# Optimization experiments

Measured on AMD Instinct MI355X. Metric: run time of the kernel, lower is better.

## Reference

```python
import jax, jax.numpy as jnp
import numpy as np

DIM = 1024
HEADS = 16
DEPTH = DIM // HEADS


def setup_inputs() -> dict:
    key = jax.random.key(0)
    ks = jax.random.split(key, 8)
    B, S = 4, 2048
    q = jax.random.normal(ks[0], (B, S, DIM), dtype=jnp.float32)
    k = jax.random.normal(ks[1], (B, S, DIM), dtype=jnp.float32)
    v = jax.random.normal(ks[2], (B, S, DIM), dtype=jnp.float32)
    # key-padding style mask: 1 = masked, 0 = attend; broadcasts over [B,H,S,S]
    mask = jax.random.randint(ks[3], (B, 1, 1, S), 0, 2).astype(jnp.float32)
    scale = 1.0 / np.sqrt(DIM)  # xavier_uniform-ish scale for square matrices
    WQ = jax.random.normal(ks[4], (DIM, DIM), dtype=jnp.float32) * scale
    WK = jax.random.normal(ks[5], (DIM, DIM), dtype=jnp.float32) * scale
    WV = jax.random.normal(ks[6], (DIM, DIM), dtype=jnp.float32) * scale
    WO = jax.random.normal(ks[7], (DIM, DIM), dtype=jnp.float32) * scale
    return {"q": q, "k": k, "v": v, "mask": mask, "WQ": WQ, "WK": WK, "WV": WV, "WO": WO}


def reference(q, k, v, mask, WQ, WK, WV, WO):
    B = q.shape[0]
    norm = jnp.asarray(np.sqrt(DEPTH), dtype=q.dtype)
    # projections -> [B,S,H,D]
    qh = (q @ WQ).reshape(B, -1, HEADS, DEPTH)
    kh = (k @ WK).reshape(B, -1, HEADS, DEPTH)
    vh = (v @ WV).reshape(B, -1, HEADS, DEPTH)
    # scores [B,H,Sq,Sk]
    g = jnp.einsum("bqhd,bkhd->bhqk", qh, kh) / norm
    g = g - mask * 1e9
    A = jax.nn.softmax(g, axis=-1)
    att = jnp.einsum("bhqk,bkhd->bqhd", A, vh).reshape(B, -1, DIM)
    return att @ WO
```

## Files before the change

### kernel.cpp

```cpp
#include <hip/hip_runtime.h>
#include <cstdint>
#include <cstddef>

#define DIM_   1024
#define HEADS_ 16
#define DEPTH_ 64
#define SEQ_   2048
#define BATCH_ 4
#define RCAP_  1152
#define NCH_   36

typedef __attribute__((ext_vector_type(8))) short short8;
typedef __attribute__((ext_vector_type(4))) float f32x4;
typedef _Float16 half8 __attribute__((ext_vector_type(8)));

__device__ __forceinline__ unsigned short f2bf(float x) {
    unsigned int u = __float_as_uint(x);
    u = u + 0x7FFFu + ((u >> 16) & 1u);
    return (unsigned short)(u >> 16);
}
__device__ __forceinline__ float bf2f(unsigned short h) {
    return __uint_as_float(((unsigned int)h) << 16);
}
__device__ __forceinline__ unsigned short f2h(float x) {
    _Float16 h = (_Float16)x;
    return __builtin_bit_cast(unsigned short, h);
}
__device__ __forceinline__ void async_cp16(const void* g, void* l) {
    __builtin_amdgcn_global_load_lds((const __attribute__((address_space(1))) void*)g,
                                     (__attribute__((address_space(3))) void*)l,
                                     16, 0, 0);
}

__global__ __launch_bounds__(64) void scan_mask(const float* __restrict__ mask,
                                                int* __restrict__ counts,
                                                int* __restrict__ idx) {
    const int b    = blockIdx.x;
    const int lane = threadIdx.x;
    const float* m = mask + (size_t)b * SEQ_;
    int* ib = idx + (size_t)b * SEQ_;
    int running = 0;
    for (int i0 = 0; i0 < SEQ_; i0 += 64) {
        const int i = i0 + lane;
        const bool keep = (m[i] == 0.0f);
        const unsigned long long bal = __ballot(keep);
        const int pre = __popcll(bal & ((1ULL << lane) - 1ULL));
        const int pos = running + pre;
        if (keep && pos < RCAP_) ib[pos] = i;
        running += __popcll(bal);
    }
    if (lane == 0) counts[b] = running < RCAP_ ? running : RCAP_;
}

__global__ __launch_bounds__(256) void convert_all(const float* __restrict__ q,
                                                   const float* __restrict__ k,
                                                   const float* __restrict__ v,
                                                   const float* __restrict__ WQ,
                                                   const float* __restrict__ WK,
                                                   const float* __restrict__ WV,
                                                   const float* __restrict__ WO,
                                                   const int* __restrict__ counts,
                                                   const int* __restrict__ idx,
                                                   unsigned short* __restrict__ qAh,
                                                   unsigned short* __restrict__ kAh,
                                                   unsigned short* __restrict__ vAh,
                                                   unsigned short* __restrict__ WhQ,
                                                   unsigned short* __restrict__ WhK,
                                                   unsigned short* __restrict__ WhV,
                                                   unsigned short* __restrict__ WhO) {
    const int bid = blockIdx.x;
    if (bid < 4096) {
        const int g  = bid * 256 + threadIdx.x;
        const int rb = g >> 14;
        const int w  = g & 16383;
        const int kt = w >> 9, x = w & 511;
        const int mtile = x >> 6, y = x & 63;
        const int kq = y >> 4, mm = y & 15;
        const int row   = rb * 128 + mtile * 16 + mm;
        const int kbase = kt * 32 + kq * 8;
        const float* src = q + (size_t)row * DIM_ + kbase;
        short8 vh;
#pragma unroll
        for (int j = 0; j < 8; ++j) vh[j] = (short)f2h(src[j]);
        *(short8*)(qAh + (size_t)g * 8) = vh;
    } else if (bid < 8704) {
        int lb = bid - 4096;
        const float* A;
        unsigned short* Ah;
        if (lb < 2304) { A = k; Ah = kAh; }
        else           { A = v; Ah = vAh; lb -= 2304; }
        const int g  = lb * 256 + threadIdx.x;
        const int rb = g >> 14;
        const int w  = g & 16383;
        const int kt = w >> 9, x = w & 511;
        const int mtile = x >> 6, y = x & 63;
        const int kq = y >> 4, mm = y & 15;
        const int b   = rb / 9;
        const int rbl = rb - b * 9;
        int r = rbl * 128 + mtile * 16 + mm;
        const int cnt = counts[b];
        if (r > cnt - 1) r = cnt - 1;
        const int rs = idx[b * SEQ_ + r];
        const int kbase = kt * 32 + kq * 8;
        const float* src = A + ((size_t)b * SEQ_ + rs) * DIM_ + kbase;
        short8 vh;
#pragma unroll
        for (int j = 0; j < 8; ++j) vh[j] = (short)f2h(src[j]);
        *(short8*)(Ah + (size_t)g * 8) = vh;
    } else {
        int lb = bid - 8704;
        const float* B;
        unsigned short* Bh;
        if (lb < 512)       { B = WQ; Bh = WhQ; }
        else if (lb < 1024) { B = WK; Bh = WhK; lb -= 512; }
        else if (lb < 1536) { B = WV; Bh = WhV; lb -= 1024; }
        else                { B = WO; Bh = WhO; lb -= 1536; }
        const int g  = lb * 256 + threadIdx.x;
        const int w  = g & 16383;
        const int kt = w >> 9, x = w & 511;
        const int nt = x >> 6, y = x & 63;
        const int kq = y >> 4, nn = y & 15;
        const int n  = nt * 16 + nn;
        const int nb = g >> 14;
        const int col = nb * 128 + n;
        const int k0 = kt * 32 + kq * 8;
        short8 vh;
#pragma unroll
        for (int j = 0; j < 8; ++j) vh[j] = (short)f2h(B[(size_t)(k0 + j) * DIM_ + col]);
        *(short8*)(Bh + (size_t)g * 8) = vh;
    }
}

__global__ __launch_bounds__(256) void gemm_qkv(const unsigned short* __restrict__ qAh,
                                                const unsigned short* __restrict__ kAh,
                                                const unsigned short* __restrict__ vAh,
                                                const unsigned short* __restrict__ WhQ,
                                                const unsigned short* __restrict__ WhK,
                                                const unsigned short* __restrict__ WhV,
                                                unsigned short* __restrict__ Qbf,
                                                unsigned short* __restrict__ Kswz,
                                                unsigned short* __restrict__ Vswz,
                                                const int* __restrict__ counts) {
    __shared__ unsigned short lds[2 * 8192];

    const int t = threadIdx.x, wave = t >> 6, lane = t & 63;
    const int x = blockIdx.x, cb = blockIdx.y;

    int mode, rb;
    const unsigned short *gA, *gB;
    unsigned short* C;
    if (x < 64)       { mode = 3; rb = x;       gA = qAh; gB = WhQ; C = Qbf; }
    else if (x < 100) { mode = 4; rb = x - 64;  gA = kAh; gB = WhK; C = Kswz; }
    else              { mode = 5; rb = x - 100; gA = vAh; gB = WhV; C = Vswz; }

    int cnt = 0, bb = 0;
    if (mode != 3) { bb = rb / 9; cnt = counts[bb]; }

    gA += (size_t)rb * 131072;
    gB += (size_t)cb * 131072;

    const int wr = wave >> 1, wc = wave & 1;

    f32x4 acc[4][4];
#pragma unroll
    for (int i = 0; i < 4; ++i)
#pragma unroll
        for (int j = 0; j < 4; ++j) acc[i][j] = (f32x4){0.f, 0.f, 0.f, 0.f};

    auto stage = [&](int kt, int sel) {
        const size_t ktO = (size_t)kt * 4096;
        char* lA = (char*)(lds + sel * 8192);
        char* lB = (char*)(lds + sel * 8192 + 4096);
#pragma unroll
        for (int i = 0; i < 2; ++i) {
            const int o = i * 4096 + t * 16;
            async_cp16((const char*)(gA + ktO) + o, lA + o);
            async_cp16((const char*)(gB + ktO) + o, lB + o);
        }
    };

    stage(0, 0);
    __syncthreads();
    int sel = 0;
    for (int kt = 0; kt < 32; ++kt) {
        if (kt < 31) stage(kt + 1, sel ^ 1);
        const unsigned short* lA = lds + sel * 8192;
        const unsigned short* lB = lA + 4096;

        half8 a[4], b[4];
#pragma unroll
        for (int i = 0; i < 4; ++i) {
            a[i] = *(const half8*)(lA + (wr * 4 + i) * 512 + lane * 8);
            b[i] = *(const half8*)(lB + (wc * 4 + i) * 512 + lane * 8);
        }
#pragma unroll
        for (int mt = 0; mt < 4; ++mt)
#pragma unroll
            for (int nt = 0; nt < 4; ++nt)
                acc[mt][nt] = __builtin_amdgcn_mfma_f32_16x16x32_f16(a[mt], b[nt], acc[mt][nt], 0, 0, 0);

        __syncthreads();
        sel ^= 1;
    }

    const int rq = lane >> 4, rc = lane & 15;
#pragma unroll
    for (int mt = 0; mt < 4; ++mt) {
#pragma unroll
        for (int nt = 0; nt < 4; ++nt) {
            const int col = cb * 128 + (wc * 4 + nt) * 16 + rc;
#pragma unroll
            for (int r = 0; r < 4; ++r) {
                const int row = rb * 128 + (wr * 4 + mt) * 16 + rq * 4 + r;
                const float val = acc[mt][nt][r];
                const int h = col >> 6, dd = col & (DEPTH_ - 1);
                if (mode == 3) {
                    const int b_ = row >> 11, s = row & (SEQ_ - 1);
                    C[((size_t)(b_ * HEADS_ + h) * SEQ_ + s) * DEPTH_ + dd] =
                        f2bf(val * 0.18033688011112042f);
                } else if (mode == 4) {
                    const int rl = row - bb * RCAP_;
                    const float sv = (rl < cnt) ? val : 0.f;
                    const size_t bh = (size_t)(bb * HEADS_ + h);
                    const size_t off = bh * (NCH_ * 2048)
                                     + (size_t)(rl >> 5) * 2048 + (size_t)((rl >> 4) & 1) * 1024
                                     + (size_t)(dd >> 5) * 512 + (size_t)((dd >> 3) & 3) * 128
                                     + (rl & 15) * 8 + (dd & 7);
                    C[off] = f2bf(sv);
                } else {
                    const int rl = row - bb * RCAP_;
                    const float sv = (rl < cnt) ? val : 0.f;
                    const size_t bh = (size_t)(bb * HEADS_ + h);
                    const size_t off = bh * (NCH_ * 2048)
                                     + (size_t)(rl >> 5) * 2048 + (size_t)(dd >> 4) * 512
                                     + (size_t)((rl >> 3) & 3) * 128
                                     + (dd & 15) * 8 + (rl & 7);
                    C[off] = f2bf(sv);
                }
            }
        }
    }
}

__global__ __launch_bounds__(256) void gemm_out(const unsigned short* __restrict__ Ah,
                                                const unsigned short* __restrict__ Bh,
                                                float* __restrict__ Cf) {
    __shared__ unsigned short lds[2 * 8192];

    const int t = threadIdx.x, wave = t >> 6, lane = t & 63;
    const int rb = blockIdx.x, cb = blockIdx.y;

    const unsigned short* gA = Ah + (size_t)rb * 131072;
    const unsigned short* gB = Bh + (size_t)cb * 131072;

    const int wr = wave >> 1, wc = wave & 1;

    f32x4 acc[4][4];
#pragma unroll
    for (int i = 0; i < 4; ++i)
#pragma unroll
        for (int j = 0; j < 4; ++j) acc[i][j] = (f32x4){0.f, 0.f, 0.f, 0.f};

    auto stage = [&](int kt, int sel) {
        const size_t ktO = (size_t)kt * 4096;
        char* lA = (char*)(lds + sel * 8192);
        char* lB = (char*)(lds + sel * 8192 + 4096);
#pragma unroll
        for (int i = 0; i < 2; ++i) {
            const int o = i * 4096 + t * 16;
            async_cp16((const char*)(gA + ktO) + o, lA + o);
            async_cp16((const char*)(gB + ktO) + o, lB + o);
        }
    };

    stage(0, 0);
    __syncthreads();
    int sel = 0;
    for (int kt = 0; kt < 32; ++kt) {
        if (kt < 31) stage(kt + 1, sel ^ 1);
        const unsigned short* lA = lds + sel * 8192;
        const unsigned short* lB = lA + 4096;

        half8 a[4], b[4];
#pragma unroll
        for (int i = 0; i < 4; ++i) {
            a[i] = *(const half8*)(lA + (wr * 4 + i) * 512 + lane * 8);
            b[i] = *(const half8*)(lB + (wc * 4 + i) * 512 + lane * 8);
        }
#pragma unroll
        for (int mt = 0; mt < 4; ++mt)
#pragma unroll
            for (int nt = 0; nt < 4; ++nt)
                acc[mt][nt] = __builtin_amdgcn_mfma_f32_16x16x32_f16(a[mt], b[nt], acc[mt][nt], 0, 0, 0);

        __syncthreads();
        sel ^= 1;
    }

    const int rq = lane >> 4, rc = lane & 15;
#pragma unroll
    for (int mt = 0; mt < 4; ++mt) {
#pragma unroll
        for (int nt = 0; nt < 4; ++nt) {
            const int col = cb * 128 + (wc * 4 + nt) * 16 + rc;
#pragma unroll
            for (int r = 0; r < 4; ++r) {
                const int row = rb * 128 + (wr * 4 + mt) * 16 + rq * 4 + r;
                Cf[(size_t)row * DIM_ + col] = acc[mt][nt][r];
            }
        }
    }
}

__global__ __launch_bounds__(256, 8) void attn_mfma(const unsigned short* __restrict__ Qbf,
                                                    const unsigned short* __restrict__ Kz,
                                                    const unsigned short* __restrict__ Vz,
                                                    const int* __restrict__ counts,
                                                    unsigned short* __restrict__ oAh) {
    __shared__ char lds[2 * 8192 + 4 * 1024];

    const int bh = blockIdx.x, qb = blockIdx.y;
    const int b = bh >> 4, h = bh & (HEADS_ - 1);
    const int t = threadIdx.x, wave = t >> 6, lane = t & 63;
    const int g = lane >> 4, n = lane & 15;
    const int cnt = counts[b];
    const int nch = (cnt + 31) >> 5;

    short8 qf[2];
    const int qrow0 = qb * 64 + wave * 16;
#pragma unroll
    for (int kf = 0; kf < 2; ++kf)
        qf[kf] = *(const short8*)(Qbf + ((size_t)bh * SEQ_ + qrow0 + n) * DEPTH_ + kf * 32 + g * 8);

    const unsigned short* Kb = Kz + (size_t)bh * NCH_ * 2048;
    const unsigned short* Vb = Vz + (size_t)bh * NCH_ * 2048;
    char* Pbase = lds + 16384 + wave * 1024;

    const int pr = n >> 1, pc = n & 1;
    int pw[2], prd;
#pragma unroll
    for (int mt = 0; mt < 2; ++mt) {
        const int G = pc * 4 + mt * 2 + (g >> 1);
        pw[mt] = pr * 128 + ((G ^ pr) << 4) + ((g & 1) << 3);
    }
    {
        const int G = pc * 4 + g;
        prd = pr * 128 + ((G ^ pr) << 4);
    }

    auto stage = [&](int c, int sel) {
        const char* gk = (const char*)(Kb + (size_t)c * 2048);
        const char* gv = (const char*)(Vb + (size_t)c * 2048);
        char* dk = lds + sel * 8192;
        async_cp16(gk + t * 16, dk + t * 16);
        async_cp16(gv + t * 16, dk + 4096 + t * 16);
    };

    f32x4 occ[4];
#pragma unroll
    for (int mt = 0; mt < 4; ++mt) occ[mt] = (f32x4){0.f, 0.f, 0.f, 0.f};
    float mrun = -3.0e38f, lsum = 0.f;

    stage(0, 0);
    __syncthreads();
    int sel = 0;
    for (int c = 0; c < nch; ++c) {
        if (c + 1 < nch) stage(c + 1, sel ^ 1);
        const char* dk = lds + sel * 8192;
        const char* dv = dk + 4096;

        short8 ka[2][2];
#pragma unroll
        for (int mt = 0; mt < 2; ++mt)
#pragma unroll
            for (int kf = 0; kf < 2; ++kf)
                ka[mt][kf] = *(const short8*)(dk + (mt * 2 + kf) * 1024 + g * 256 + n * 16);

        f32x4 sacc[2];
#pragma unroll
        for (int mt = 0; mt < 2; ++mt) {
            sacc[mt] = (f32x4){0.f, 0.f, 0.f, 0.f};
#pragma unroll
            for (int kf = 0; kf < 2; ++kf)
                sacc[mt] = __builtin_amdgcn_mfma_f32_16x16x32_bf16(ka[mt][kf], qf[kf], sacc[mt], 0, 0, 0);
        }

        float sv[8];
#pragma unroll
        for (int mt = 0; mt < 2; ++mt)
#pragma unroll
            for (int r = 0; r < 4; ++r) sv[mt * 4 + r] = sacc[mt][r];
        if (c == nch - 1 && (cnt & 31)) {
#pragma unroll
            for (int mt = 0; mt < 2; ++mt)
#pragma unroll
                for (int r = 0; r < 4; ++r)
                    if (c * 32 + mt * 16 + g * 4 + r >= cnt) sv[mt * 4 + r] = -3.0e38f;
        }

        float mc = fmaxf(fmaxf(fmaxf(sv[0], sv[1]), fmaxf(sv[2], sv[3])),
                         fmaxf(fmaxf(sv[4], sv[5]), fmaxf(sv[6], sv[7])));
        mc = fmaxf(mc, __shfl_xor(mc, 16, 64));
        mc = fmaxf(mc, __shfl_xor(mc, 32, 64));

        if (!__all(mc <= mrun + 8.0f)) {
            const float mn = fmaxf(mrun, mc);
            const float alpha = __builtin_amdgcn_exp2f(mrun - mn);
#pragma unroll
            for (int mt = 0; mt < 4; ++mt)
#pragma unroll
                for (int r = 0; r < 4; ++r) occ[mt][r] *= alpha;
            lsum *= alpha;
            mrun = mn;
        }

        float p[8];
#pragma unroll
        for (int i = 0; i < 8; ++i) p[i] = __builtin_amdgcn_exp2f(sv[i] - mrun);
        float ps = ((p[0] + p[1]) + (p[2] + p[3])) + ((p[4] + p[5]) + (p[6] + p[7]));
        ps += __shfl_xor(ps, 16, 64);
        ps += __shfl_xor(ps, 32, 64);
        lsum += ps;

        unsigned int pk[4];
#pragma unroll
        for (int i = 0; i < 4; ++i) {
            unsigned int r_;
            asm("v_cvt_pk_bf16_f32 %0, %1, %2" : "=v"(r_) : "v"(p[2 * i]), "v"(p[2 * i + 1]));
            pk[i] = r_;
        }
#pragma unroll
        for (int mt = 0; mt < 2; ++mt)
            *(uint2*)(Pbase + pw[mt]) = make_uint2(pk[mt * 2], pk[mt * 2 + 1]);
        const short8 pf = *(const short8*)(Pbase + prd);

        short8 va[4];
#pragma unroll
        for (int mt = 0; mt < 4; ++mt)
            va[mt] = *(const short8*)(dv + mt * 1024 + g * 256 + n * 16);
#pragma unroll
        for (int mt = 0; mt < 4; ++mt)
            occ[mt] = __builtin_amdgcn_mfma_f32_16x16x32_bf16(va[mt], pf, occ[mt], 0, 0, 0);

        __syncthreads();
        sel ^= 1;
    }

    const float inv = 1.0f / lsum;
    const int row = b * SEQ_ + qrow0 + n;
    const size_t rbase = (size_t)(row >> 7) * 131072 + (size_t)((row >> 4) & 7) * 512
                       + (size_t)(row & 15) * 8 + (g & 1) * 4;
#pragma unroll
    for (int mt = 0; mt < 4; ++mt) {
        const int kt_ = h * 2 + (mt >> 1);
        const int kq_ = (mt * 2 + (g >> 1)) & 3;
        const unsigned int lo = (unsigned int)f2h(occ[mt][0] * inv) | ((unsigned int)f2h(occ[mt][1] * inv) << 16);
        const unsigned int hi = (unsigned int)f2h(occ[mt][2] * inv) | ((unsigned int)f2h(occ[mt][3] * inv) << 16);
        *(uint2*)(oAh + rbase + (size_t)kt_ * 4096 + (size_t)kq_ * 128) = make_uint2(lo, hi);
    }
}

extern "C" void kernel_launch(void* const* d_in, const int* in_sizes, int n_in,
                              void* d_out, int out_size, void* d_ws, size_t ws_size,
                              hipStream_t stream) {
    const float* q    = (const float*)d_in[0];
    const float* k    = (const float*)d_in[1];
    const float* v    = (const float*)d_in[2];
    const float* mask = (const float*)d_in[3];
    const float* WQ   = (const float*)d_in[4];
    const float* WK   = (const float*)d_in[5];
    const float* WV   = (const float*)d_in[6];
    const float* WO   = (const float*)d_in[7];
    float* out = (float*)d_out;

    const size_t MiB = 1048576;
    if (ws_size < 104 * MiB) return;

    char* W = (char*)d_ws;
    int*   counts = (int*)W;
    int*   idx    = counts + 16;
    unsigned short* Qbf  = (unsigned short*)(W + 1 * MiB);
    unsigned short* Kswz = (unsigned short*)(W + 18 * MiB);
    unsigned short* Vswz = (unsigned short*)(W + 28 * MiB);
    unsigned short* oAh  = (unsigned short*)(W + 38 * MiB);
    unsigned short* qAh  = (unsigned short*)(W + 56 * MiB);
    unsigned short* kAh  = (unsigned short*)(W + 74 * MiB);
    unsigned short* vAh  = (unsigned short*)(W + 84 * MiB);
    unsigned short* WhQ  = (unsigned short*)(W + 94 * MiB);
    unsigned short* WhK  = (unsigned short*)(W + 96 * MiB);
    unsigned short* WhV  = (unsigned short*)(W + 98 * MiB);
    unsigned short* WhO  = (unsigned short*)(W + 100 * MiB);

    scan_mask<<<BATCH_, 64, 0, stream>>>(mask, counts, idx);

    convert_all<<<10752, 256, 0, stream>>>(q, k, v, WQ, WK, WV, WO, counts, idx,
                                           qAh, kAh, vAh, WhQ, WhK, WhV, WhO);

    gemm_qkv<<<dim3(136, 8), 256, 0, stream>>>(qAh, kAh, vAh, WhQ, WhK, WhV,
                                               Qbf, Kswz, Vswz, counts);

    attn_mfma<<<dim3(BATCH_ * HEADS_, SEQ_ / 64), 256, 0, stream>>>(Qbf, Kswz, Vswz, counts, oAh);

    gemm_out<<<dim3(64, 8), 256, 0, stream>>>(oAh, WhO, out);
}
```

Before: 322.9 us.

## Permute K row layout so P fragments feed PV MFMA directly from registers

```diff
diff --git a/kernel.cpp b/kernel.cpp
--- a/kernel.cpp
+++ b/kernel.cpp
@@ -18,9 +18,6 @@
     unsigned int u = __float_as_uint(x);
     u = u + 0x7FFFu + ((u >> 16) & 1u);
     return (unsigned short)(u >> 16);
-}
-__device__ __forceinline__ float bf2f(unsigned short h) {
-    return __uint_as_float(((unsigned int)h) << 16);
 }
 __device__ __forceinline__ unsigned short f2h(float x) {
     _Float16 h = (_Float16)x;
@@ -222,10 +219,13 @@
                     const int rl = row - bb * RCAP_;
                     const float sv = (rl < cnt) ? val : 0.f;
                     const size_t bh = (size_t)(bb * HEADS_ + h);
+                    const int u    = rl & 31;
+                    const int mtn  = (u >> 2) & 1;
+                    const int rowi = ((u >> 3) << 2) + (u & 3);
                     const size_t off = bh * (NCH_ * 2048)
-                                     + (size_t)(rl >> 5) * 2048 + (size_t)((rl >> 4) & 1) * 1024
+                                     + (size_t)(rl >> 5) * 2048 + (size_t)mtn * 1024
                                      + (size_t)(dd >> 5) * 512 + (size_t)((dd >> 3) & 3) * 128
-                                     + (rl & 15) * 8 + (dd & 7);
+                                     + rowi * 8 + (dd & 7);
                     C[off] = f2bf(sv);
                 } else {
                     const int rl = row - bb * RCAP_;
@@ -317,7 +317,7 @@
                                                     const unsigned short* __restrict__ Vz,
                                                     const int* __restrict__ counts,
                                                     unsigned short* __restrict__ oAh) {
-    __shared__ char lds[2 * 8192 + 4 * 1024];
+    __shared__ char lds[2 * 8192];
 
     const int bh = blockIdx.x, qb = blockIdx.y;
     const int b = bh >> 4, h = bh & (HEADS_ - 1);
@@ -334,19 +334,6 @@
 
     const unsigned short* Kb = Kz + (size_t)bh * NCH_ * 2048;
     const unsigned short* Vb = Vz + (size_t)bh * NCH_ * 2048;
-    char* Pbase = lds + 16384 + wave * 1024;
-
-    const int pr = n >> 1, pc = n & 1;
-    int pw[2], prd;
-#pragma unroll
-    for (int mt = 0; mt < 2; ++mt) {
-        const int G = pc * 4 + mt * 2 + (g >> 1);
-        pw[mt] = pr * 128 + ((G ^ pr) << 4) + ((g & 1) << 3);
-    }
-    {
-        const int G = pc * 4 + g;
-        prd = pr * 128 + ((G ^ pr) << 4);
-    }
 
     auto stage = [&](int c, int sel) {
         const char* gk = (const char*)(Kb + (size_t)c * 2048);
@@ -395,7 +382,7 @@
             for (int mt = 0; mt < 2; ++mt)
 #pragma unroll
                 for (int r = 0; r < 4; ++r)
-                    if (c * 32 + mt * 16 + g * 4 + r >= cnt) sv[mt * 4 + r] = -3.0e38f;
+                    if (c * 32 + g * 8 + mt * 4 + r >= cnt) sv[mt * 4 + r] = -3.0e38f;
         }
 
         float mc = fmaxf(fmaxf(fmaxf(sv[0], sv[1]), fmaxf(sv[2], sv[3])),
@@ -422,17 +409,14 @@
         ps += __shfl_xor(ps, 32, 64);
         lsum += ps;
 
-        unsigned int pk[4];
-#pragma unroll
-        for (int i = 0; i < 4; ++i) {
-            unsigned int r_;
-            asm("v_cvt_pk_bf16_f32 %0, %1, %2" : "=v"(r_) : "v"(p[2 * i]), "v"(p[2 * i + 1]));
-            pk[i] = r_;
-        }
-#pragma unroll
-        for (int mt = 0; mt < 2; ++mt)
-            *(uint2*)(Pbase + pw[mt]) = make_uint2(pk[mt * 2], pk[mt * 2 + 1]);
-        const short8 pf = *(const short8*)(Pbase + prd);
+        unsigned int pk0, pk1, pk2, pk3;
+        asm("v_cvt_pk_bf16_f32 %0, %1, %2" : "=v"(pk0) : "v"(p[0]), "v"(p[1]));
+        asm("v_cvt_pk_bf16_f32 %0, %1, %2" : "=v"(pk1) : "v"(p[2]), "v"(p[3]));
+        asm("v_cvt_pk_bf16_f32 %0, %1, %2" : "=v"(pk2) : "v"(p[4]), "v"(p[5]));
+        asm("v_cvt_pk_bf16_f32 %0, %1, %2" : "=v"(pk3) : "v"(p[6]), "v"(p[7]));
+        int4 wf;
+        wf.x = (int)pk0; wf.y = (int)pk1; wf.z = (int)pk2; wf.w = (int)pk3;
+        const short8 pf = __builtin_bit_cast(short8, wf);
 
         short8 va[4];
 #pragma unroll
```

Result: faster. 309.0 us (-4.3%).
